# Kernel optimization log

Hardware: AMD Instinct MI355X
Metric: run time of the kernel (lower is better)

Reference implementation:

```python
import math
import jax, jax.numpy as jnp
import numpy as np

B, S, D, H, V = 8, 1024, 512, 8, 32000
HD = D // H


def _position_embedding(seq_len, d_model):
    pos = jnp.arange(seq_len, dtype=jnp.float32)[:, None]                 # [S,1]
    div = jnp.exp(jnp.arange(0, d_model, 2, dtype=jnp.float32) * (-math.log(10000.0) / d_model))  # [D/2]
    ang = pos * div                                                        # [S,D/2]
    # interleave sin (even cols) / cos (odd cols)
    return jnp.stack([jnp.sin(ang), jnp.cos(ang)], axis=-1).reshape(seq_len, d_model)


def _min_max_normalize(w):
    lo = jnp.min(w, axis=-1, keepdims=True)
    hi = jnp.max(w, axis=-1, keepdims=True)
    return (w - lo) / (hi - lo)


def _converable_mask(h, Wc, bc):
    bs, seq = h.shape[0], h.shape[1]
    half = seq // 2
    shift = math.ceil(seq / 2)
    width = jnp.einsum('bsd,od->bso', h, Wc)[..., 0] + bc[0]               # [B,S]
    width = _min_max_normalize(width)[..., None]                           # [B,S,1]
    origin = jnp.concatenate([jnp.linspace(1.0, 0.0, half),
                              jnp.linspace(0.0, 1.0, seq - half)])         # [S]
    origin_mask = 1.0 - jax.nn.sigmoid((origin[None, None, :] - width) * 100.0)  # [B,S,S]
    idx = (jnp.arange(seq - 1, -1, -1)[:, None] + jnp.arange(seq)[None, :]) % seq  # [S,S]
    idx = jnp.roll(idx, shift, axis=0)
    # torch.roll of a [1,S] row along dim 0 is a no-op
    cmp = idx >= jnp.arange(seq)[None, :]                                  # [S,S] bool
    move = jnp.concatenate([cmp[:shift], ~cmp[shift:]], axis=0)            # [S,S]
    gathered = jnp.take_along_axis(origin_mask, idx[None, :, :], axis=2)   # [B,S,S]
    return gathered * move.astype(origin_mask.dtype)


def setup_inputs():
    key = jax.random.key(0)
    ks = jax.random.split(key, 9)
    s_emb = 1.0
    s_hd = 1.0 / math.sqrt(HD)
    s_d = 1.0 / math.sqrt(D)
    return {
        'x':   jax.random.randint(ks[0], (B, S), 0, V),
        'emb': jax.random.normal(ks[1], (V, D), dtype=jnp.float32) * s_emb,
        'Wq':  jax.random.normal(ks[2], (HD, HD), dtype=jnp.float32) * s_hd,
        'Wk':  jax.random.normal(ks[3], (HD, HD), dtype=jnp.float32) * s_hd,
        'Wv':  jax.random.normal(ks[4], (HD, HD), dtype=jnp.float32) * s_hd,
        'Wo':  jax.random.normal(ks[5], (D, D), dtype=jnp.float32) * s_d,
        'bo':  jnp.zeros((D,), dtype=jnp.float32),
        'Wc':  jax.random.normal(ks[6], (1, D), dtype=jnp.float32) * s_d,
        'bc':  jnp.zeros((1,), dtype=jnp.float32),
    }


def reference(x, emb, Wq, Wk, Wv, Wo, bo, Wc, bc):
    h = emb[x] + _position_embedding(S, D)[None]                           # [B,S,D]
    mask = _converable_mask(h, Wc, bc)                                     # [B,S,S]
    hh = h.reshape(B, S, H, HD)
    q = jnp.einsum('bshd,od->bsho', hh, Wq)
    k = jnp.einsum('bshd,od->bsho', hh, Wk)
    v = jnp.einsum('bshd,od->bsho', hh, Wv)
    energy = jnp.einsum('bqhd,bkhd->bhqk', q, k)                           # [B,H,S,S]
    # mask [B,S,S] broadcasts as [1,B,S,S]; valid because B == H (as in original)
    energy = energy * mask
    attn = jax.nn.softmax(energy / math.sqrt(D), axis=3)
    out = jnp.einsum('bhqk,bkhd->bqhd', attn, v).reshape(B, S, D)
    out = out @ Wo.T + bo
    return (out, mask)
```

## Files before the change

### kernel.cpp

```cpp
#include <hip/hip_runtime.h>
#include <hip/hip_bf16.h>
#include <math.h>

#define Bn 8
#define Sn 1024
#define Dn 512
#define Hn 8
#define HDn 64

typedef __bf16 bf16x8 __attribute__((ext_vector_type(8)));
typedef __bf16 bf16x4 __attribute__((ext_vector_type(4)));
typedef __bf16 bf16x2 __attribute__((ext_vector_type(2)));
typedef float  f32x4  __attribute__((ext_vector_type(4)));
typedef float  f32x16 __attribute__((ext_vector_type(16)));
typedef unsigned int u32x4 __attribute__((ext_vector_type(4)));

__device__ __forceinline__ unsigned enc_f(float v) {
    unsigned u = __float_as_uint(v);
    return (u & 0x80000000u) ? ~u : (u | 0x80000000u);
}
__device__ __forceinline__ float dec_f(unsigned k) {
    unsigned u = (k & 0x80000000u) ? (k ^ 0x80000000u) : ~k;
    return __uint_as_float(u);
}

__global__ __launch_bounds__(256) void k_fused(
        const int* __restrict__ x, const float* __restrict__ emb,
        const float* __restrict__ Wc, const float* __restrict__ bc,
        const float* __restrict__ Wq, const float* __restrict__ Wk,
        const float* __restrict__ Wv,
        float* __restrict__ width, unsigned* __restrict__ lohi,
        __bf16* __restrict__ q, __bf16* __restrict__ k, __bf16* __restrict__ vt) {
    __shared__ __align__(16) __bf16 Xs[64][72];
    __shared__ __align__(16) __bf16 WqS[64][72];
    __shared__ __align__(16) __bf16 WkS[64][72];
    __shared__ __align__(16) __bf16 WvS[64][72];
    __shared__ float wtok[8];
    int t = threadIdx.x;
    int bs0 = blockIdx.x * 8;
    int m0 = blockIdx.x * 64;
    int w = t >> 6, lane = t & 63, quad = lane >> 4, li = lane & 15;

    {
        int token = t >> 5, l32 = t & 31;
        int bs = bs0 + token;
        int s = bs & (Sn - 1);
        int tok = x[bs];
        float wpart = 0.f;
        int row = token * 8 + ((l32 * 16) >> 6);
        #pragma unroll
        for (int j = 0; j < 4; ++j) {
            int d0 = l32 * 16 + j * 4;
            float4 ev = *(const float4*)&emb[(size_t)tok * Dn + d0];
            float4 wc = *(const float4*)&Wc[d0];
            float hv[4];
            #pragma unroll
            for (int i = 0; i < 4; ++i) {
                int d = d0 + i;
                float f = __expf((float)(d & ~1) * (-9.210340371976184f / 512.0f));
                float ang = (float)s * f;
                float pe = (d & 1) ? __cosf(ang) : __sinf(ang);
                hv[i] = (&ev.x)[i] + pe;
                wpart += hv[i] * (&wc.x)[i];
            }
            *(bf16x4*)&Xs[row][d0 & 63] =
                (bf16x4){(__bf16)hv[0], (__bf16)hv[1], (__bf16)hv[2], (__bf16)hv[3]};
        }
        #pragma unroll
        for (int off = 1; off < 32; off <<= 1) wpart += __shfl_xor(wpart, off);
        if (l32 == 0) { float wv = wpart + bc[0]; width[bs] = wv; wtok[token] = wv; }
    }
    #pragma unroll
    for (int it = 0; it < 4; ++it) {
        int e = (it * 256 + t) * 4; int r = e >> 6, c = e & 63;
        float4 qv = *(const float4*)&Wq[e];
        *(bf16x4*)&WqS[r][c] = (bf16x4){(__bf16)qv.x, (__bf16)qv.y, (__bf16)qv.z, (__bf16)qv.w};
        float4 kv = *(const float4*)&Wk[e];
        *(bf16x4*)&WkS[r][c] = (bf16x4){(__bf16)kv.x, (__bf16)kv.y, (__bf16)kv.z, (__bf16)kv.w};
        float4 vv = *(const float4*)&Wv[e];
        *(bf16x4*)&WvS[r][c] = (bf16x4){(__bf16)vv.x, (__bf16)vv.y, (__bf16)vv.z, (__bf16)vv.w};
    }
    __syncthreads();

    if (t == 0) {
        float mn = wtok[0], mx = wtok[0];
        #pragma unroll
        for (int i = 1; i < 8; ++i) { mn = fminf(mn, wtok[i]); mx = fmaxf(mx, wtok[i]); }
        int b = bs0 >> 10;
        atomicMin(&lohi[b], enc_f(mn));
        atomicMin(&lohi[8 + b], ~enc_f(mx));
    }

    bf16x8 A0 = *(const bf16x8*)&Xs[w * 16 + li][quad * 8];
    bf16x8 A1 = *(const bf16x8*)&Xs[w * 16 + li][32 + quad * 8];
    f32x4 aq[4], ak[4], av[4];
    #pragma unroll
    for (int n = 0; n < 4; ++n) {
        aq[n] = (f32x4){0.f,0.f,0.f,0.f}; ak[n] = aq[n]; av[n] = aq[n];
        bf16x8 Bq0 = *(const bf16x8*)&WqS[n * 16 + li][quad * 8];
        bf16x8 Bq1 = *(const bf16x8*)&WqS[n * 16 + li][32 + quad * 8];
        aq[n] = __builtin_amdgcn_mfma_f32_16x16x32_bf16(A0, Bq0, aq[n], 0, 0, 0);
        aq[n] = __builtin_amdgcn_mfma_f32_16x16x32_bf16(A1, Bq1, aq[n], 0, 0, 0);
        bf16x8 Bk0 = *(const bf16x8*)&WkS[n * 16 + li][quad * 8];
        bf16x8 Bk1 = *(const bf16x8*)&WkS[n * 16 + li][32 + quad * 8];
        ak[n] = __builtin_amdgcn_mfma_f32_16x16x32_bf16(A0, Bk0, ak[n], 0, 0, 0);
        ak[n] = __builtin_amdgcn_mfma_f32_16x16x32_bf16(A1, Bk1, ak[n], 0, 0, 0);
        bf16x8 Bv0 = *(const bf16x8*)&WvS[n * 16 + li][quad * 8];
        bf16x8 Bv1 = *(const bf16x8*)&WvS[n * 16 + li][32 + quad * 8];
        av[n] = __builtin_amdgcn_mfma_f32_16x16x32_bf16(A0, Bv0, av[n], 0, 0, 0);
        av[n] = __builtin_amdgcn_mfma_f32_16x16x32_bf16(A1, Bv1, av[n], 0, 0, 0);
    }

    const float SCALE = 0.04419417382415922f;
    __syncthreads();
    #pragma unroll
    for (int n = 0; n < 4; ++n)
        #pragma unroll
        for (int r = 0; r < 4; ++r) {
            int row = w * 16 + quad * 4 + r, col = n * 16 + li;
            WkS[row][col] = (__bf16)(aq[n][r] * SCALE);
            WvS[row][col] = (__bf16)ak[n][r];
            WqS[row][col] = (__bf16)av[n][r];
        }
    __syncthreads();

    {
        int row = t >> 2, part = (t & 3) * 16;
        int Rg = m0 + row;
        int bsI = Rg >> 3, head = Rg & 7;
        int bq = bsI >> 10, sq = bsI & (Sn - 1);
        size_t base = (((size_t)(bq * Hn + head)) * Sn + sq) * HDn + part;
        *(bf16x8*)&q[base]     = *(bf16x8*)&WkS[row][part];
        *(bf16x8*)&q[base + 8] = *(bf16x8*)&WkS[row][part + 8];
        *(bf16x8*)&k[base]     = *(bf16x8*)&WvS[row][part];
        *(bf16x8*)&k[base + 8] = *(bf16x8*)&WvS[row][part + 8];
    }

    __bf16 (*Vs)[72] = WqS;
    int bs0i = m0 >> 3;
    int b = bs0i >> 10, s0l = bs0i & (Sn - 1);
    #pragma unroll
    for (int i = 0; i < 2; ++i) {
        int p = t + 256 * i;
        int head = p >> 6, o = p & 63;
        __bf16 tmp[8];
        #pragma unroll
        for (int j = 0; j < 8; ++j) tmp[j] = Vs[j * 8 + head][o];
        *(bf16x8*)&vt[(((size_t)(b * Hn + head)) * HDn + o) * Sn + s0l] = *(bf16x8*)tmp;
    }
}

__global__ void k_mask(const float* __restrict__ width, const unsigned* __restrict__ lohi,
                       float* __restrict__ mask_out) {
    int bs = blockIdx.x;
    int b = bs >> 10;
    int s = bs & (Sn - 1);
    float lo = dec_f(lohi[b]);
    float hi = dec_f(~lohi[8 + b]);
    float wn = (width[bs] - lo) / (hi - lo);
    for (int t = threadIdx.x; t < Sn; t += 256) {
        int it = (t - s + 1535) & (Sn - 1);
        float origin = (it < 512) ? (1.0f - (float)it * (1.0f / 511.0f))
                                  : ((float)(it - 512) * (1.0f / 511.0f));
        float z = (origin - wn) * 100.0f;
        float om;
        if (z >= 0.0f) { float e = __expf(-z); om = e / (1.0f + e); }
        else           { float e = __expf(z);  om = 1.0f / (1.0f + e); }
        bool cmpv = (it >= t);
        bool mv = (s < 512) ? cmpv : !cmpv;
        mask_out[(size_t)bs * Sn + t] = mv ? om : 0.0f;
    }
}

__global__ __launch_bounds__(128, 2) void k_attn(
        const __bf16* __restrict__ q, const __bf16* __restrict__ k,
        const __bf16* __restrict__ vt, const float* __restrict__ mask,
        __bf16* __restrict__ ao) {
    __shared__ __align__(16) __bf16 Ks[2][64][72];
    __shared__ __align__(16) __bf16 Vt[2][64][72];
    int blk = blockIdx.x;
    int hh = blk & 7;
    int qt = (blk >> 3) & 15;
    int b  = blk >> 7;
    int bh = b * Hn + hh;
    int q0 = qt * 64;
    int t = threadIdx.x;
    int w = t >> 6, lane = t & 63, hi5 = lane >> 5, l31 = lane & 31;

    const __bf16* qbase  = q  + ((size_t)bh * Sn + q0 + w * 32) * HDn;
    const __bf16* kbase  = k  + (size_t)bh * Sn * HDn;
    const __bf16* vtbase = vt + (size_t)bh * HDn * Sn;
    const float* mq = mask + ((size_t)hh * Sn + q0 + w * 32 + l31) * Sn;

    bf16x8 Qf[4];
    #pragma unroll
    for (int c = 0; c < 4; ++c)
        Qf[c] = *(const bf16x8*)&qbase[(size_t)l31 * HDn + c * 16 + hi5 * 8];

    int sr = t >> 3, sc = (t & 7) * 8;
    bf16x8 pk[4], pv[4];
    #pragma unroll
    for (int j = 0; j < 4; ++j) {
        pk[j] = *(const bf16x8*)&kbase[(size_t)(sr + j * 16) * HDn + sc];
        pv[j] = *(const bf16x8*)&vtbase[(size_t)(sr + j * 16) * Sn + sc];
    }
    #pragma unroll
    for (int j = 0; j < 4; ++j) {
        *(bf16x8*)&Ks[0][sr + j * 16][sc] = pk[j];
        *(bf16x8*)&Vt[0][sr + j * 16][sc] = pv[j];
    }
    __syncthreads();

    f32x16 OT[2];
    OT[0] = (f32x16){0.f,0.f,0.f,0.f,0.f,0.f,0.f,0.f,0.f,0.f,0.f,0.f,0.f,0.f,0.f,0.f};
    OT[1] = OT[0];
    float rs = 0.f;

    for (int ti = 0; ti < 16; ++ti) {
        int cur = ti & 1;

        float4 mk[2][4];
        #pragma unroll
        for (int kg = 0; kg < 2; ++kg)
            #pragma unroll
            for (int g = 0; g < 4; ++g)
                mk[kg][g] = *(const float4*)&mq[ti * 64 + kg * 32 + g * 8 + hi5 * 4];

        if (ti < 15) {
            int k0n = (ti + 1) * 64;
            #pragma unroll
            for (int j = 0; j < 4; ++j) {
                pk[j] = *(const bf16x8*)&kbase[(size_t)(k0n + sr + j * 16) * HDn + sc];
                pv[j] = *(const bf16x8*)&vtbase[(size_t)(sr + j * 16) * Sn + k0n + sc];
            }
        }

        f32x16 St[2];
        St[0] = (f32x16){0.f,0.f,0.f,0.f,0.f,0.f,0.f,0.f,0.f,0.f,0.f,0.f,0.f,0.f,0.f,0.f};
        St[1] = St[0];
        __builtin_amdgcn_s_setprio(1);
        #pragma unroll
        for (int c = 0; c < 4; ++c) {
            bf16x8 K0 = *(const bf16x8*)&Ks[cur][l31][c * 16 + hi5 * 8];
            St[0] = __builtin_amdgcn_mfma_f32_32x32x16_bf16(K0, Qf[c], St[0], 0, 0, 0);
            bf16x8 K1 = *(const bf16x8*)&Ks[cur][32 + l31][c * 16 + hi5 * 8];
            St[1] = __builtin_amdgcn_mfma_f32_32x32x16_bf16(K1, Qf[c], St[1], 0, 0, 0);
        }
        __builtin_amdgcn_s_setprio(0);

        unsigned pkd[2][4][2];
        #pragma unroll
        for (int kg = 0; kg < 2; ++kg) {
            #pragma unroll
            for (int g = 0; g < 4; ++g) {
                float p0 = __expf(St[kg][4 * g + 0] * mk[kg][g].x);
                float p1 = __expf(St[kg][4 * g + 1] * mk[kg][g].y);
                float p2 = __expf(St[kg][4 * g + 2] * mk[kg][g].z);
                float p3 = __expf(St[kg][4 * g + 3] * mk[kg][g].w);
                rs += (p0 + p1) + (p2 + p3);
                bf16x2 plo = { (__bf16)p0, (__bf16)p1 };
                bf16x2 phi = { (__bf16)p2, (__bf16)p3 };
                pkd[kg][g][0] = __builtin_bit_cast(unsigned, plo);
                pkd[kg][g][1] = __builtin_bit_cast(unsigned, phi);
            }
        }

        __builtin_amdgcn_s_setprio(1);
        #pragma unroll
        for (int c = 0; c < 4; ++c) {
            const int kg = c >> 1, gA = 2 * (c & 1), gB = gA + 1;
            unsigned z0 = hi5 ? pkd[kg][gB][0] : pkd[kg][gA][0];
            unsigned z1 = hi5 ? pkd[kg][gB][1] : pkd[kg][gA][1];
            unsigned y0 = hi5 ? pkd[kg][gA][0] : pkd[kg][gB][0];
            unsigned y1 = hi5 ? pkd[kg][gA][1] : pkd[kg][gB][1];
            unsigned x0 = (unsigned)__shfl_xor((int)y0, 32);
            unsigned x1 = (unsigned)__shfl_xor((int)y1, 32);
            u32x4 du;
            du[0] = hi5 ? x0 : z0;
            du[1] = hi5 ? x1 : z1;
            du[2] = hi5 ? z0 : x0;
            du[3] = hi5 ? z1 : x1;
            bf16x8 Pf = __builtin_bit_cast(bf16x8, du);
            bf16x8 V0 = *(const bf16x8*)&Vt[cur][l31][c * 16 + hi5 * 8];
            OT[0] = __builtin_amdgcn_mfma_f32_32x32x16_bf16(V0, Pf, OT[0], 0, 0, 0);
            bf16x8 V1 = *(const bf16x8*)&Vt[cur][32 + l31][c * 16 + hi5 * 8];
            OT[1] = __builtin_amdgcn_mfma_f32_32x32x16_bf16(V1, Pf, OT[1], 0, 0, 0);
        }
        __builtin_amdgcn_s_setprio(0);

        if (ti < 15) {
            #pragma unroll
            for (int j = 0; j < 4; ++j) {
                *(bf16x8*)&Ks[cur ^ 1][sr + j * 16][sc] = pk[j];
                *(bf16x8*)&Vt[cur ^ 1][sr + j * 16][sc] = pv[j];
            }
            __syncthreads();
        }
    }

    rs += __shfl_xor(rs, 32);
    float inv = __fdividef(1.0f, rs);

    size_t orow = ((size_t)b * Sn + q0 + w * 32 + l31) * Dn + hh * HDn;
    #pragma unroll
    for (int og = 0; og < 2; ++og)
        #pragma unroll
        for (int g2 = 0; g2 < 4; ++g2) {
            bf16x4 ov = { (__bf16)(OT[og][4 * g2 + 0] * inv),
                          (__bf16)(OT[og][4 * g2 + 1] * inv),
                          (__bf16)(OT[og][4 * g2 + 2] * inv),
                          (__bf16)(OT[og][4 * g2 + 3] * inv) };
            *(bf16x4*)&ao[orow + og * 32 + g2 * 8 + hi5 * 4] = ov;
        }
}

__global__ __launch_bounds__(256) void k_proj(
        const __bf16* __restrict__ ao, const float* __restrict__ Wo,
        const float* __restrict__ bo, float* __restrict__ out) {
    __shared__ __align__(16) __bf16 As[64][72];
    __shared__ __align__(16) __bf16 Bs[64][72];
    __shared__ __align__(16) float  Os[64][68];
    int bm = blockIdx.x >> 3;
    int bn = blockIdx.x & 7;
    int m0 = bm * 64, n0 = bn * 64;
    int t = threadIdx.x;
    int w = t >> 6, lane = t & 63, quad = lane >> 4, li = lane & 15;

    f32x4 O[4];
    #pragma unroll
    for (int n = 0; n < 4; ++n) O[n] = (f32x4){0.f, 0.f, 0.f, 0.f};

    for (int k0 = 0; k0 < Dn; k0 += 64) {
        if (k0) __syncthreads();
        #pragma unroll
        for (int it = 0; it < 2; ++it) {
            int e = (it * 256 + t) * 8; int r = e >> 6, c = e & 63;
            *(bf16x8*)&As[r][c] = *(const bf16x8*)&ao[(size_t)(m0 + r) * Dn + k0 + c];
        }
        #pragma unroll
        for (int it = 0; it < 4; ++it) {
            int e = (it * 256 + t) * 4; int r = e >> 6, c = e & 63;
            float4 wv = *(const float4*)&Wo[(size_t)(n0 + r) * Dn + k0 + c];
            *(bf16x4*)&Bs[r][c] = (bf16x4){(__bf16)wv.x, (__bf16)wv.y, (__bf16)wv.z, (__bf16)wv.w};
        }
        __syncthreads();

        bf16x8 A0 = *(const bf16x8*)&As[w * 16 + li][quad * 8];
        bf16x8 A1 = *(const bf16x8*)&As[w * 16 + li][32 + quad * 8];
        #pragma unroll
        for (int n = 0; n < 4; ++n) {
            bf16x8 B0 = *(const bf16x8*)&Bs[n * 16 + li][quad * 8];
            O[n] = __builtin_amdgcn_mfma_f32_16x16x32_bf16(A0, B0, O[n], 0, 0, 0);
            bf16x8 B1 = *(const bf16x8*)&Bs[n * 16 + li][32 + quad * 8];
            O[n] = __builtin_amdgcn_mfma_f32_16x16x32_bf16(A1, B1, O[n], 0, 0, 0);
        }
    }

    #pragma unroll
    for (int n = 0; n < 4; ++n) {
        float bias = bo[n0 + n * 16 + li];
        #pragma unroll
        for (int r = 0; r < 4; ++r)
            Os[w * 16 + quad * 4 + r][n * 16 + li] = O[n][r] + bias;
    }
    __syncthreads();
    {
        int row = t >> 2, part = (t & 3) * 16;
        size_t base = (size_t)(m0 + row) * Dn + n0 + part;
        #pragma unroll
        for (int j = 0; j < 4; ++j)
            *(float4*)&out[base + j * 4] = *(const float4*)&Os[row][part + j * 4];
    }
}

extern "C" void kernel_launch(void* const* d_in, const int* in_sizes, int n_in,
                              void* d_out, int out_size, void* d_ws, size_t ws_size,
                              hipStream_t stream) {
    const int*   x   = (const int*)d_in[0];
    const float* emb = (const float*)d_in[1];
    const float* Wq  = (const float*)d_in[2];
    const float* Wk  = (const float*)d_in[3];
    const float* Wv  = (const float*)d_in[4];
    const float* Wo  = (const float*)d_in[5];
    const float* bo  = (const float*)d_in[6];
    const float* Wc  = (const float*)d_in[7];
    const float* bc  = (const float*)d_in[8];

    float* ws      = (float*)d_ws;
    float* width   = ws;
    unsigned* lohi = (unsigned*)(width + Bn * Sn);
    __bf16* qb   = (__bf16*)(ws + Bn * Sn + 16);
    __bf16* kb   = qb + (size_t)Bn * Sn * Dn;
    __bf16* vtb  = kb + (size_t)Bn * Sn * Dn;
    __bf16* ao   = vtb + (size_t)Bn * Sn * Dn;

    float* out      = (float*)d_out;
    float* mask_out = out + (size_t)Bn * Sn * Dn;

    hipMemsetAsync(lohi, 0xFF, 16 * sizeof(unsigned), stream);
    k_fused<<<(Bn * Sn) / 8, 256, 0, stream>>>(x, emb, Wc, bc, Wq, Wk, Wv,
                                               width, lohi, qb, kb, vtb);
    k_mask<<<Bn * Sn, 256, 0, stream>>>(width, lohi, mask_out);
    k_attn<<<Bn * Hn * (Sn / 64), 128, 0, stream>>>(qb, kb, vtb, mask_out, ao);
    k_proj<<<(Bn * Sn / 64) * (Dn / 64), 256, 0, stream>>>(ao, Wo, bo, out);
}
```

Measured before the change: 221.6 us.

## Widen attention blocks to 128 queries, preload LDS fragments, use permlane32 swap

The attention kernel now runs 256 threads (4 waves) per block, each block covering 128 query rows, so every K/V tile staged in LDS serves twice as many queries. Each thread loads half as many K/V vectors per tile. All K and V MFMA fragments for a tile are read from LDS into registers before the compute phase. The shuffle-plus-select sequence for repacking P is replaced by permlane32_swap. This raises register pressure and halves the block count, which may reduce occupancy or wave-level parallelism.

```diff
diff --git a/kernel.cpp b/kernel.cpp
--- a/kernel.cpp
+++ b/kernel.cpp
@@ -14,6 +14,7 @@
 typedef float  f32x4  __attribute__((ext_vector_type(4)));
 typedef float  f32x16 __attribute__((ext_vector_type(16)));
 typedef unsigned int u32x4 __attribute__((ext_vector_type(4)));
+typedef int i32x2 __attribute__((ext_vector_type(2)));
 
 __device__ __forceinline__ unsigned enc_f(float v) {
     unsigned u = __float_as_uint(v);
@@ -172,7 +173,7 @@
     }
 }
 
-__global__ __launch_bounds__(128, 2) void k_attn(
+__global__ __launch_bounds__(256, 2) void k_attn(
         const __bf16* __restrict__ q, const __bf16* __restrict__ k,
         const __bf16* __restrict__ vt, const float* __restrict__ mask,
         __bf16* __restrict__ ao) {
@@ -180,10 +181,10 @@
     __shared__ __align__(16) __bf16 Vt[2][64][72];
     int blk = blockIdx.x;
     int hh = blk & 7;
-    int qt = (blk >> 3) & 15;
-    int b  = blk >> 7;
+    int qt = (blk >> 3) & 7;
+    int b  = blk >> 6;
     int bh = b * Hn + hh;
-    int q0 = qt * 64;
+    int q0 = qt * 128;
     int t = threadIdx.x;
     int w = t >> 6, lane = t & 63, hi5 = lane >> 5, l31 = lane & 31;
 
@@ -197,18 +198,16 @@
     for (int c = 0; c < 4; ++c)
         Qf[c] = *(const bf16x8*)&qbase[(size_t)l31 * HDn + c * 16 + hi5 * 8];
 
-    int sr = t >> 3, sc = (t & 7) * 8;
-    bf16x8 pk[4], pv[4];
-    #pragma unroll
-    for (int j = 0; j < 4; ++j) {
-        pk[j] = *(const bf16x8*)&kbase[(size_t)(sr + j * 16) * HDn + sc];
-        pv[j] = *(const bf16x8*)&vtbase[(size_t)(sr + j * 16) * Sn + sc];
-    }
-    #pragma unroll
-    for (int j = 0; j < 4; ++j) {
-        *(bf16x8*)&Ks[0][sr + j * 16][sc] = pk[j];
-        *(bf16x8*)&Vt[0][sr + j * 16][sc] = pv[j];
-    }
+    int sr0 = t >> 3, sc0 = (t & 7) * 8;
+    bf16x8 pk0, pk1, pv0, pv1;
+    pk0 = *(const bf16x8*)&kbase[(size_t)sr0 * HDn + sc0];
+    pk1 = *(const bf16x8*)&kbase[(size_t)(sr0 + 32) * HDn + sc0];
+    pv0 = *(const bf16x8*)&vtbase[(size_t)sr0 * Sn + sc0];
+    pv1 = *(const bf16x8*)&vtbase[(size_t)(sr0 + 32) * Sn + sc0];
+    *(bf16x8*)&Ks[0][sr0][sc0] = pk0;
+    *(bf16x8*)&Ks[0][sr0 + 32][sc0] = pk1;
+    *(bf16x8*)&Vt[0][sr0][sc0] = pv0;
+    *(bf16x8*)&Vt[0][sr0 + 32][sc0] = pv1;
     __syncthreads();
 
     f32x16 OT[2];
@@ -228,12 +227,23 @@
 
         if (ti < 15) {
             int k0n = (ti + 1) * 64;
+            pk0 = *(const bf16x8*)&kbase[(size_t)(k0n + sr0) * HDn + sc0];
+            pk1 = *(const bf16x8*)&kbase[(size_t)(k0n + sr0 + 32) * HDn + sc0];
+            pv0 = *(const bf16x8*)&vtbase[(size_t)sr0 * Sn + k0n + sc0];
+            pv1 = *(const bf16x8*)&vtbase[(size_t)(sr0 + 32) * Sn + k0n + sc0];
+        }
+
+        bf16x8 Kf[2][4], Vf[2][4];
+        #pragma unroll
+        for (int h = 0; h < 2; ++h)
             #pragma unroll
-            for (int j = 0; j < 4; ++j) {
-                pk[j] = *(const bf16x8*)&kbase[(size_t)(k0n + sr + j * 16) * HDn + sc];
-                pv[j] = *(const bf16x8*)&vtbase[(size_t)(sr + j * 16) * Sn + k0n + sc];
-            }
-        }
+            for (int c = 0; c < 4; ++c)
+                Kf[h][c] = *(const bf16x8*)&Ks[cur][h * 32 + l31][c * 16 + hi5 * 8];
+        #pragma unroll
+        for (int h = 0; h < 2; ++h)
+            #pragma unroll
+            for (int c = 0; c < 4; ++c)
+                Vf[h][c] = *(const bf16x8*)&Vt[cur][h * 32 + l31][c * 16 + hi5 * 8];
 
         f32x16 St[2];
         St[0] = (f32x16){0.f,0.f,0.f,0.f,0.f,0.f,0.f,0.f,0.f,0.f,0.f,0.f,0.f,0.f,0.f,0.f};
@@ -241,10 +251,8 @@
         __builtin_amdgcn_s_setprio(1);
         #pragma unroll
         for (int c = 0; c < 4; ++c) {
-            bf16x8 K0 = *(const bf16x8*)&Ks[cur][l31][c * 16 + hi5 * 8];
-            St[0] = __builtin_amdgcn_mfma_f32_32x32x16_bf16(K0, Qf[c], St[0], 0, 0, 0);
-            bf16x8 K1 = *(const bf16x8*)&Ks[cur][32 + l31][c * 16 + hi5 * 8];
-            St[1] = __builtin_amdgcn_mfma_f32_32x32x16_bf16(K1, Qf[c], St[1], 0, 0, 0);
+            St[0] = __builtin_amdgcn_mfma_f32_32x32x16_bf16(Kf[0][c], Qf[c], St[0], 0, 0, 0);
+            St[1] = __builtin_amdgcn_mfma_f32_32x32x16_bf16(Kf[1][c], Qf[c], St[1], 0, 0, 0);
         }
         __builtin_amdgcn_s_setprio(0);
 
@@ -269,31 +277,26 @@
         #pragma unroll
         for (int c = 0; c < 4; ++c) {
             const int kg = c >> 1, gA = 2 * (c & 1), gB = gA + 1;
-            unsigned z0 = hi5 ? pkd[kg][gB][0] : pkd[kg][gA][0];
-            unsigned z1 = hi5 ? pkd[kg][gB][1] : pkd[kg][gA][1];
-            unsigned y0 = hi5 ? pkd[kg][gA][0] : pkd[kg][gB][0];
-            unsigned y1 = hi5 ? pkd[kg][gA][1] : pkd[kg][gB][1];
-            unsigned x0 = (unsigned)__shfl_xor((int)y0, 32);
-            unsigned x1 = (unsigned)__shfl_xor((int)y1, 32);
+            i32x2 r0 = __builtin_amdgcn_permlane32_swap(
+                (int)pkd[kg][gA][0], (int)pkd[kg][gB][0], false, false);
+            i32x2 r1 = __builtin_amdgcn_permlane32_swap(
+                (int)pkd[kg][gA][1], (int)pkd[kg][gB][1], false, false);
             u32x4 du;
-            du[0] = hi5 ? x0 : z0;
-            du[1] = hi5 ? x1 : z1;
-            du[2] = hi5 ? z0 : x0;
-            du[3] = hi5 ? z1 : x1;
+            du[0] = (unsigned)r0[0];
+            du[1] = (unsigned)r1[0];
+            du[2] = (unsigned)r0[1];
+            du[3] = (unsigned)r1[1];
             bf16x8 Pf = __builtin_bit_cast(bf16x8, du);
-            bf16x8 V0 = *(const bf16x8*)&Vt[cur][l31][c * 16 + hi5 * 8];
-            OT[0] = __builtin_amdgcn_mfma_f32_32x32x16_bf16(V0, Pf, OT[0], 0, 0, 0);
-            bf16x8 V1 = *(const bf16x8*)&Vt[cur][32 + l31][c * 16 + hi5 * 8];
-            OT[1] = __builtin_amdgcn_mfma_f32_32x32x16_bf16(V1, Pf, OT[1], 0, 0, 0);
+            OT[0] = __builtin_amdgcn_mfma_f32_32x32x16_bf16(Vf[0][c], Pf, OT[0], 0, 0, 0);
+            OT[1] = __builtin_amdgcn_mfma_f32_32x32x16_bf16(Vf[1][c], Pf, OT[1], 0, 0, 0);
         }
         __builtin_amdgcn_s_setprio(0);
 
         if (ti < 15) {
-            #pragma unroll
-            for (int j = 0; j < 4; ++j) {
-                *(bf16x8*)&Ks[cur ^ 1][sr + j * 16][sc] = pk[j];
-                *(bf16x8*)&Vt[cur ^ 1][sr + j * 16][sc] = pv[j];
-            }
+            *(bf16x8*)&Ks[cur ^ 1][sr0][sc0] = pk0;
+            *(bf16x8*)&Ks[cur ^ 1][sr0 + 32][sc0] = pk1;
+            *(bf16x8*)&Vt[cur ^ 1][sr0][sc0] = pv0;
+            *(bf16x8*)&Vt[cur ^ 1][sr0 + 32][sc0] = pv1;
             __syncthreads();
         }
     }
@@ -401,6 +404,6 @@
     k_fused<<<(Bn * Sn) / 8, 256, 0, stream>>>(x, emb, Wc, bc, Wq, Wk, Wv,
                                                width, lohi, qb, kb, vtb);
     k_mask<<<Bn * Sn, 256, 0, stream>>>(width, lohi, mask_out);
-    k_attn<<<Bn * Hn * (Sn / 64), 128, 0, stream>>>(qb, kb, vtb, mask_out, ao);
+    k_attn<<<Bn * Hn * (Sn / 128), 256, 0, stream>>>(qb, kb, vtb, mask_out, ao);
     k_proj<<<(Bn * Sn / 64) * (Dn / 64), 256, 0, stream>>>(ao, Wo, bo, out);
 }
```

After: 216.7 us. 1.02x faster.
